# Optimization experiments

Measured on AMD Instinct MI355X. Metric: run time of the kernel, lower is better.

The kernel has to match this reference:

```python
import jax, jax.numpy as jnp
import numpy as np

K = 3  # kernel_dim
PAD = 1


def setup_inputs() -> dict:
    key = jax.random.key(0)
    ks = jax.random.split(key, 7)
    B, C_in, C_out, R = 2, 32, 64, 64
    H = W = D = 64
    return {
        "x": jax.random.normal(ks[0], (B, C_in, H, W, D), dtype=jnp.float32),
        "U_k_h": jax.random.normal(ks[1], (K, R), dtype=jnp.float32),
        "U_k_w": jax.random.normal(ks[2], (K, R), dtype=jnp.float32),
        "U_k_d": jax.random.normal(ks[3], (K, R), dtype=jnp.float32),
        "U_c_in": jax.random.normal(ks[4], (C_in, R), dtype=jnp.float32),
        "U_c_out": jax.random.normal(ks[5], (R, C_out), dtype=jnp.float32),
        "bias": jax.random.normal(ks[6], (C_out,), dtype=jnp.float32),
    }


def _cpd_conv3d(x, U_k_h, U_k_w, U_k_d, U_c_in, U_c_out, bias):
    # Equivalent to: patches[b,c,h,w,d,kh,kw,kd] contracted with
    # U_c_in[c,r] U_k_h[kh,r] U_k_w[kw,r] U_k_d[kd,r] U_c_out[r,co]
    # -> out[b,co,h,w,d].  We exploit the CP (rank-separable) structure
    # instead of materializing the unfolded patch tensor.
    xp = jnp.pad(x, ((0, 0), (0, 0), (PAD, PAD), (PAD, PAD), (PAD, PAD)))
    # channel contraction: [B, R, H+2, W+2, D+2]
    t = jnp.einsum('bchwd,cr->brhwd', xp, U_c_in)
    B, R, Hp, Wp, Dp = t.shape
    H, W, D = Hp - 2 * PAD, Wp - 2 * PAD, Dp - 2 * PAD
    # separable kernel contractions (fixed K=3 unrolled loops)
    t = sum(t[:, :, k:k + H, :, :] * U_k_h[k][None, :, None, None, None] for k in range(K))
    t = sum(t[:, :, :, k:k + W, :] * U_k_w[k][None, :, None, None, None] for k in range(K))
    t = sum(t[:, :, :, :, k:k + D] * U_k_d[k][None, :, None, None, None] for k in range(K))
    out = jnp.einsum('brhwd,rc->bchwd', t, U_c_out)
    return out + bias[None, :, None, None, None]


def reference(x, U_k_h, U_k_w, U_k_d, U_c_in, U_c_out, bias):
    return _cpd_conv3d(x, U_k_h, U_k_w, U_k_d, U_c_in, U_c_out, bias)
```

## Files before the change

### kernel.cpp

```cpp
#include <hip/hip_runtime.h>
#include <hip/hip_bf16.h>

typedef __attribute__((ext_vector_type(8))) short short8;
typedef __attribute__((ext_vector_type(4))) float f32x4;

__device__ __forceinline__ float b2f(short s) {
    return __uint_as_float(((unsigned int)(unsigned short)s) << 16);
}
__device__ __forceinline__ short f2b(float f) {
    unsigned int u = __float_as_uint(f);
    u += 0x7fffu + ((u >> 16) & 1u);
    return (short)(u >> 16);
}
__device__ __forceinline__ unsigned pack2(float a, float b) {
    return (unsigned)(unsigned short)f2b(a) | ((unsigned)(unsigned short)f2b(b) << 16);
}

__global__ __launch_bounds__(256)
void k1_channel(const float* __restrict__ x,
                const float* __restrict__ Ucin,
                short* __restrict__ t)
{
    __shared__ float xs[128 * 36];
    const int tid  = threadIdx.x;
    const int bid  = blockIdx.x;
    const int b    = bid >> 11;
    const int sp0  = (bid & 2047) << 7;
    const float* xb = x + ((long)b << 23) + sp0;

    const int lane = tid & 63;
    const int wv   = tid >> 6;

    float u[32];
#pragma unroll
    for (int c = 0; c < 32; ++c) u[c] = Ucin[c * 64 + lane];

    for (int i = tid; i < 2048; i += 256) {
        int c2 = i >> 7;
        int so = i & 127;
        float a0 = xb[((long)(2 * c2)     << 18) + so];
        float a1 = xb[((long)(2 * c2 + 1) << 18) + so];
        float2 v; v.x = a0; v.y = a1;
        *(float2*)&xs[so * 36 + 2 * c2] = v;
    }
    __syncthreads();

    short* tb = t + (((size_t)b << 18) + sp0) * 64 + lane;
    for (int s = 0; s < 32; ++s) {
        const int so = wv * 32 + s;
        const float4* row = (const float4*)&xs[so * 36];
        float a0 = 0.f, a1 = 0.f;
#pragma unroll
        for (int k = 0; k < 8; ++k) {
            float4 xx = row[k];
            a0 += xx.x * u[4 * k + 0];
            a1 += xx.y * u[4 * k + 1];
            a0 += xx.z * u[4 * k + 2];
            a1 += xx.w * u[4 * k + 3];
        }
        tb[(size_t)so * 64] = f2b(a0 + a1);
    }
}

__global__ __launch_bounds__(256)
void k2_conv_gemm(const short* __restrict__ t,
                  const float* __restrict__ Ukh,
                  const float* __restrict__ Ukw,
                  const float* __restrict__ Ukd,
                  const float* __restrict__ Uco,
                  const float* __restrict__ bias,
                  float* __restrict__ out)
{
    __shared__ short s[66 * 64];
    __shared__ short p[64 * 72];
    __shared__ short ucot[64 * 72];

    const int tid = threadIdx.x;

    const int bid  = blockIdx.x;
    const int slot = bid & 7;
    const int idx  = bid >> 3;
    const int b    = idx >> 9;
    const int rem  = idx & 511;
    const int h    = slot * 8 + (rem >> 6);
    const int w    = rem & 63;

    const short* colp[9];
    bool valid[9];
#pragma unroll
    for (int kh = 0; kh < 3; ++kh) {
#pragma unroll
        for (int kw = 0; kw < 3; ++kw) {
            int hh = h + kh - 1, ww = w + kw - 1;
            bool v = ((unsigned)hh < 64u) && ((unsigned)ww < 64u);
            valid[kh * 3 + kw] = v;
            long base = v ? ((long)(b * 262144 + hh * 4096 + ww * 64) << 6) : 0;
            colp[kh * 3 + kw] = t + base;
        }
    }

    for (int i = tid; i < 4096; i += 256) {
        int r = i >> 6, co = i & 63;
        ucot[co * 72 + r] = f2b(Uco[i]);
    }

    const int rq = tid & 15;
    float4 W[9];
    {
        float4 a[3], c[3];
#pragma unroll
        for (int k = 0; k < 3; ++k) {
            a[k] = *(const float4*)&Ukh[k * 64 + 4 * rq];
            c[k] = *(const float4*)&Ukw[k * 64 + 4 * rq];
        }
#pragma unroll
        for (int kh = 0; kh < 3; ++kh)
#pragma unroll
            for (int kw = 0; kw < 3; ++kw) {
                int kk = kh * 3 + kw;
                float m = valid[kk] ? 1.f : 0.f;
                W[kk].x = a[kh].x * c[kw].x * m;
                W[kk].y = a[kh].y * c[kw].y * m;
                W[kk].z = a[kh].z * c[kw].z * m;
                W[kk].w = a[kh].w * c[kw].w * m;
            }
    }
    for (int it = tid; it < 66 * 16; it += 256) {
        int sd = it >> 4;
        int d  = sd - 1;
        float a0 = 0.f, a1 = 0.f, a2 = 0.f, a3 = 0.f;
        if ((unsigned)d < 64u) {
            int off = d * 64 + 4 * rq;
#pragma unroll
            for (int kk = 0; kk < 9; ++kk) {
                uint2 uu = *(const uint2*)(colp[kk] + off);
                a0 += W[kk].x * b2f((short)(uu.x));
                a1 += W[kk].y * b2f((short)(uu.x >> 16));
                a2 += W[kk].z * b2f((short)(uu.y));
                a3 += W[kk].w * b2f((short)(uu.y >> 16));
            }
        }
        uint2 o; o.x = pack2(a0, a1); o.y = pack2(a2, a3);
        *(uint2*)&s[sd * 64 + 4 * rq] = o;
    }
    __syncthreads();

    {
        float4 Wd[3];
#pragma unroll
        for (int k = 0; k < 3; ++k)
            Wd[k] = *(const float4*)&Ukd[k * 64 + 4 * rq];
        for (int u = tid; u < 64 * 16; u += 256) {
            int d = u >> 4;
            float a0 = 0.f, a1 = 0.f, a2 = 0.f, a3 = 0.f;
#pragma unroll
            for (int k = 0; k < 3; ++k) {
                uint2 uu = *(const uint2*)&s[(d + k) * 64 + 4 * rq];
                a0 += Wd[k].x * b2f((short)(uu.x));
                a1 += Wd[k].y * b2f((short)(uu.x >> 16));
                a2 += Wd[k].z * b2f((short)(uu.y));
                a3 += Wd[k].w * b2f((short)(uu.y >> 16));
            }
            uint2 o; o.x = pack2(a0, a1); o.y = pack2(a2, a3);
            *(uint2*)&p[d * 72 + 4 * rq] = o;
        }
    }
    __syncthreads();

    {
        const int lane = tid & 63, wv = tid >> 6;
        const int l15 = lane & 15, quad = lane >> 4;
        short8 afr0 = *(const short8*)&p[(wv * 16 + l15) * 72 + quad * 8];
        short8 afr1 = *(const short8*)&p[(wv * 16 + l15) * 72 + 32 + quad * 8];
        f32x4 acc[4] = {};
#pragma unroll
        for (int nt = 0; nt < 4; ++nt) {
            short8 b0 = *(const short8*)&ucot[(nt * 16 + l15) * 72 + quad * 8];
            short8 b1 = *(const short8*)&ucot[(nt * 16 + l15) * 72 + 32 + quad * 8];
            acc[nt] = __builtin_amdgcn_mfma_f32_16x16x32_bf16(afr0, b0, acc[nt], 0, 0, 0);
            acc[nt] = __builtin_amdgcn_mfma_f32_16x16x32_bf16(afr1, b1, acc[nt], 0, 0, 0);
        }
#pragma unroll
        for (int nt = 0; nt < 4; ++nt) {
            int co = nt * 16 + l15;
            float bs = bias[co];
            int d = wv * 16 + quad * 4;
            float4 o;
            o.x = acc[nt][0] + bs; o.y = acc[nt][1] + bs;
            o.z = acc[nt][2] + bs; o.w = acc[nt][3] + bs;
            long addr = ((long)(b * 64 + co) << 18) + (h << 12) + (w << 6) + d;
            *(float4*)&out[addr] = o;
        }
    }
}

#define NTH 512
#define NPADP 656
#define SMEM_BYTES ((NPADP*32 + NPADP*32 + 432*32 + 64*32 + 64*64)*2 + 576*4)

__global__ __launch_bounds__(NTH)
void cpd_conv3d_fused_fb(const float* __restrict__ x,
                         const float* __restrict__ Ukh,
                         const float* __restrict__ Ukw,
                         const float* __restrict__ Ukd,
                         const float* __restrict__ Ucin,
                         const float* __restrict__ Uco,
                         const float* __restrict__ bias,
                         float* __restrict__ out)
{
    extern __shared__ char smem[];
    short* xs   = (short*)smem;
    short* t0   = xs   + NPADP*32;
    short* t1   = t0   + NPADP*32;
    short* uct  = t1   + 432*32;
    short* ucot = uct  + 64*32;
    float* ukf  = (float*)(ucot + 64*64);

    const int tid  = threadIdx.x;
    const int lane = tid & 63;
    const int wv   = tid >> 6;
    const int l15  = lane & 15;
    const int quad = lane >> 4;
    const int rg   = tid & 3;

    const int bid = blockIdx.x;
    const int dt = bid & 3, wt = (bid >> 2) & 15, ht = (bid >> 6) & 15, b = bid >> 10;
    const int h0 = ht * 4, w0 = wt * 4, d0 = dt * 16;

    for (int i = tid; i < 576; i += NTH) {
        float v = (i < 192) ? Ukh[i] : (i < 384 ? Ukw[i - 192] : Ukd[i - 384]);
        ukf[i] = v;
    }
    for (int i = tid; i < 2048; i += NTH) {
        int r = i >> 5, c = i & 31;
        uct[i] = f2b(Ucin[c * 64 + r]);
    }
    for (int i = tid; i < 4096; i += NTH) {
        int co = i >> 6, r = i & 63;
        ucot[i] = f2b(Uco[r * 64 + co]);
    }
    for (int i = tid; i < NPADP * 32; i += NTH) {
        int pp = i >> 5, c = i & 31;
        float v = 0.f;
        if (pp < 648) {
            int ph = pp / 108, rem = pp - ph * 108;
            int pw = rem / 18, pd = rem - pw * 18;
            int gh = h0 + ph - 1, gw = w0 + pw - 1, gd = d0 + pd - 1;
            if ((unsigned)gh < 64u && (unsigned)gw < 64u && (unsigned)gd < 64u)
                v = x[((long)(b * 32 + c) << 18) + (gh << 12) + (gw << 6) + gd];
        }
        xs[i] = f2b(v);
    }
    __syncthreads();

    f32x4 acc[8] = {};

    for (int pass = 0; pass < 2; ++pass) {
        const int rbase = pass * 32;
        {
            const int nt = wv & 1;
            short8 bfrag = *(const short8*)&uct[(rbase + nt * 16 + l15) * 32 + quad * 8];
            for (int mt = (wv >> 1); mt <= 40; mt += 4) {
                short8 afrag = *(const short8*)&xs[(mt * 16 + l15) * 32 + quad * 8];
                f32x4 c = {};
                c = __builtin_amdgcn_mfma_f32_16x16x32_bf16(afrag, bfrag, c, 0, 0, 0);
                const int col = nt * 16 + l15;
#pragma unroll
                for (int i2 = 0; i2 < 4; ++i2)
                    t0[(mt * 16 + quad * 4 + i2) * 32 + col] = f2b(c[i2]);
            }
        }
        __syncthreads();
        {
            float wh[3][8];
#pragma unroll
            for (int k = 0; k < 3; ++k) {
                const float4* pp_ = (const float4*)&ukf[k * 64 + rbase + rg * 8];
                float4 u0 = pp_[0], u1 = pp_[1];
                wh[k][0]=u0.x; wh[k][1]=u0.y; wh[k][2]=u0.z; wh[k][3]=u0.w;
                wh[k][4]=u1.x; wh[k][5]=u1.y; wh[k][6]=u1.z; wh[k][7]=u1.w;
            }
            for (int item = tid; item < 1728; item += NTH) {
                int q = item >> 2;
                float v[8] = {};
#pragma unroll
                for (int k = 0; k < 3; ++k) {
                    short8 sv = *(const short8*)&t0[(q + k * 108) * 32 + rg * 8];
#pragma unroll
                    for (int j = 0; j < 8; ++j) v[j] += wh[k][j] * b2f(sv[j]);
                }
                short8 o;
#pragma unroll
                for (int j = 0; j < 8; ++j) o[j] = f2b(v[j]);
                *(short8*)&t1[q * 32 + rg * 8] = o;
            }
        }
        __syncthreads();
        {
            float ww[3][8];
#pragma unroll
            for (int k = 0; k < 3; ++k) {
                const float4* pp_ = (const float4*)&ukf[(3 + k) * 64 + rbase + rg * 8];
                float4 u0 = pp_[0], u1 = pp_[1];
                ww[k][0]=u0.x; ww[k][1]=u0.y; ww[k][2]=u0.z; ww[k][3]=u0.w;
                ww[k][4]=u1.x; ww[k][5]=u1.y; ww[k][6]=u1.z; ww[k][7]=u1.w;
            }
            for (int item = tid; item < 1152; item += NTH) {
                int q2 = item >> 2;
                int oh = q2 / 72;
                int src = q2 + oh * 36;
                float v[8] = {};
#pragma unroll
                for (int k = 0; k < 3; ++k) {
                    short8 sv = *(const short8*)&t1[(src + k * 18) * 32 + rg * 8];
#pragma unroll
                    for (int j = 0; j < 8; ++j) v[j] += ww[k][j] * b2f(sv[j]);
                }
                short8 o;
#pragma unroll
                for (int j = 0; j < 8; ++j) o[j] = f2b(v[j]);
                *(short8*)&t0[q2 * 32 + rg * 8] = o;
            }
        }
        __syncthreads();
        {
            float wd[3][8];
#pragma unroll
            for (int k = 0; k < 3; ++k) {
                const float4* pp_ = (const float4*)&ukf[(6 + k) * 64 + rbase + rg * 8];
                float4 u0 = pp_[0], u1 = pp_[1];
                wd[k][0]=u0.x; wd[k][1]=u0.y; wd[k][2]=u0.z; wd[k][3]=u0.w;
                wd[k][4]=u1.x; wd[k][5]=u1.y; wd[k][6]=u1.z; wd[k][7]=u1.w;
            }
            for (int item = tid; item < 1024; item += NTH) {
                int pq = item >> 2;
                int src = pq + (pq >> 4) * 2;
                float v[8] = {};
#pragma unroll
                for (int k = 0; k < 3; ++k) {
                    short8 sv = *(const short8*)&t0[(src + k) * 32 + rg * 8];
#pragma unroll
                    for (int j = 0; j < 8; ++j) v[j] += wd[k][j] * b2f(sv[j]);
                }
                short8 o;
#pragma unroll
                for (int j = 0; j < 8; ++j) o[j] = f2b(v[j]);
                *(short8*)&t1[pq * 32 + rg * 8] = o;
            }
        }
        __syncthreads();
        {
            short8 bfr[4];
#pragma unroll
            for (int nt = 0; nt < 4; ++nt)
                bfr[nt] = *(const short8*)&ucot[(nt * 16 + l15) * 64 + rbase + quad * 8];
#pragma unroll
            for (int i = 0; i < 8; ++i) {
                int mt = wv * 2 + (i >> 2), nt = i & 3;
                short8 afr = *(const short8*)&t1[(mt * 16 + l15) * 32 + quad * 8];
                acc[i] = __builtin_amdgcn_mfma_f32_16x16x32_bf16(afr, bfr[nt], acc[i], 0, 0, 0);
            }
        }
    }

#pragma unroll
    for (int i = 0; i < 8; ++i) {
        int mt = wv * 2 + (i >> 2), nt = i & 3;
        int co = nt * 16 + l15;
        int oh = mt >> 2, ow = mt & 3;
        float bs = bias[co];
        float4 o4;
        o4.x = acc[i][0] + bs; o4.y = acc[i][1] + bs;
        o4.z = acc[i][2] + bs; o4.w = acc[i][3] + bs;
        long addr = ((long)(b * 64 + co) << 18) + ((long)(h0 + oh) << 12)
                  + ((w0 + ow) << 6) + (d0 + quad * 4);
        *(float4*)&out[addr] = o4;
    }
}

extern "C" void kernel_launch(void* const* d_in, const int* in_sizes, int n_in,
                              void* d_out, int out_size, void* d_ws, size_t ws_size,
                              hipStream_t stream) {
    const float* x    = (const float*)d_in[0];
    const float* Ukh  = (const float*)d_in[1];
    const float* Ukw  = (const float*)d_in[2];
    const float* Ukd  = (const float*)d_in[3];
    const float* Ucin = (const float*)d_in[4];
    const float* Uco  = (const float*)d_in[5];
    const float* bias = (const float*)d_in[6];
    float* out = (float*)d_out;

    const size_t needed = (size_t)2 * 262144 * 64 * 2;
    if (ws_size >= needed) {
        short* t = (short*)d_ws;
        k1_channel<<<4096, 256, 0, stream>>>(x, Ucin, t);
        k2_conv_gemm<<<8192, 256, 0, stream>>>(t, Ukh, Ukw, Ukd, Uco, bias, out);
    } else {
        (void)hipFuncSetAttribute((const void*)cpd_conv3d_fused_fb,
                                  hipFuncAttributeMaxDynamicSharedMemorySize,
                                  SMEM_BYTES);
        cpd_conv3d_fused_fb<<<2048, NTH, SMEM_BYTES, stream>>>(
            x, Ukh, Ukw, Ukd, Ucin, Uco, bias, out);
    }
}
```

Baseline: 292.5 us.

## Precompute bf16 transposed U_c_out once and software-pipeline k2 HW-stage loads

Adds a tiny prep kernel that converts and transposes U_c_out into bf16 in workspace once, so each of the 8192 k2 blocks copies it with 16-byte vector loads instead of converting 4096 floats with strided stores. The HW-combine stage is restructured into a fixed 4-iteration loop with register double-buffering of the nine column loads, and zero halo rows are written separately. This aims to hide global load latency and trim per-block setup, at the cost of more registers and an extra launch.

```diff
diff --git a/kernel.cpp b/kernel.cpp
--- a/kernel.cpp
+++ b/kernel.cpp
@@ -14,6 +14,14 @@
 }
 __device__ __forceinline__ unsigned pack2(float a, float b) {
     return (unsigned)(unsigned short)f2b(a) | ((unsigned)(unsigned short)f2b(b) << 16);
+}
+
+__global__ __launch_bounds__(64)
+void k0_prep(const float* __restrict__ Uco, short* __restrict__ ucotT)
+{
+    const int i  = blockIdx.x * 64 + threadIdx.x;
+    const int co = i >> 6, r = i & 63;
+    ucotT[co * 64 + r] = f2b(Uco[r * 64 + co]);
 }
 
 __global__ __launch_bounds__(256)
@@ -69,6 +77,7 @@
                   const float* __restrict__ Ukd,
                   const float* __restrict__ Uco,
                   const float* __restrict__ bias,
+                  const short* __restrict__ ucotT,
                   float* __restrict__ out)
 {
     __shared__ short s[66 * 64];
@@ -99,9 +108,17 @@
         }
     }
 
-    for (int i = tid; i < 4096; i += 256) {
-        int r = i >> 6, co = i & 63;
-        ucot[co * 72 + r] = f2b(Uco[i]);
+    if (ucotT) {
+        for (int i = tid; i < 512; i += 256) {
+            int co = i >> 3, rb = i & 7;
+            short8 v = *(const short8*)&ucotT[co * 64 + rb * 8];
+            *(short8*)&ucot[co * 72 + rb * 8] = v;
+        }
+    } else {
+        for (int i = tid; i < 4096; i += 256) {
+            int r = i >> 6, co = i & 63;
+            ucot[co * 72 + r] = f2b(Uco[i]);
+        }
     }
 
     const int rq = tid & 15;
@@ -125,23 +142,46 @@
                 W[kk].w = a[kh].w * c[kw].w * m;
             }
     }
-    for (int it = tid; it < 66 * 16; it += 256) {
-        int sd = it >> 4;
-        int d  = sd - 1;
-        float a0 = 0.f, a1 = 0.f, a2 = 0.f, a3 = 0.f;
-        if ((unsigned)d < 64u) {
-            int off = d * 64 + 4 * rq;
+
+    if (tid < 32) {
+        int sd = (tid < 16) ? 0 : 65;
+        int rr = tid & 15;
+        uint2 z; z.x = 0u; z.y = 0u;
+        *(uint2*)&s[sd * 64 + 4 * rr] = z;
+    }
+
+    {
+        const int off0 = (tid >> 4) * 64 + 4 * rq;
+        uint2 cur[9];
+#pragma unroll
+        for (int kk = 0; kk < 9; ++kk)
+            cur[kk] = *(const uint2*)(colp[kk] + off0);
+
+#pragma unroll
+        for (int j = 0; j < 4; ++j) {
+            uint2 nxt[9];
+            if (j < 3) {
+#pragma unroll
+                for (int kk = 0; kk < 9; ++kk)
+                    nxt[kk] = *(const uint2*)(colp[kk] + off0 + 1024 * (j + 1));
+            }
+            float a0 = 0.f, a1 = 0.f, a2 = 0.f, a3 = 0.f;
 #pragma unroll
             for (int kk = 0; kk < 9; ++kk) {
-                uint2 uu = *(const uint2*)(colp[kk] + off);
+                uint2 uu = cur[kk];
                 a0 += W[kk].x * b2f((short)(uu.x));
                 a1 += W[kk].y * b2f((short)(uu.x >> 16));
                 a2 += W[kk].z * b2f((short)(uu.y));
                 a3 += W[kk].w * b2f((short)(uu.y >> 16));
             }
-        }
-        uint2 o; o.x = pack2(a0, a1); o.y = pack2(a2, a3);
-        *(uint2*)&s[sd * 64 + 4 * rq] = o;
+            int sd = 1 + (tid >> 4) + 16 * j;
+            uint2 o; o.x = pack2(a0, a1); o.y = pack2(a2, a3);
+            *(uint2*)&s[sd * 64 + 4 * rq] = o;
+            if (j < 3) {
+#pragma unroll
+                for (int kk = 0; kk < 9; ++kk) cur[kk] = nxt[kk];
+            }
+        }
     }
     __syncthreads();
 
@@ -390,11 +430,17 @@
     const float* bias = (const float*)d_in[6];
     float* out = (float*)d_out;
 
-    const size_t needed = (size_t)2 * 262144 * 64 * 2;
-    if (ws_size >= needed) {
+    const size_t needT = (size_t)2 * 262144 * 64 * 2;
+    const size_t needM = 4096 * 2;
+    if (ws_size >= needT) {
         short* t = (short*)d_ws;
+        short* ucotT = nullptr;
+        if (ws_size >= needT + needM) {
+            ucotT = (short*)((char*)d_ws + needT);
+            k0_prep<<<64, 64, 0, stream>>>(Uco, ucotT);
+        }
         k1_channel<<<4096, 256, 0, stream>>>(x, Ucin, t);
-        k2_conv_gemm<<<8192, 256, 0, stream>>>(t, Ukh, Ukw, Ukd, Uco, bias, out);
+        k2_conv_gemm<<<8192, 256, 0, stream>>>(t, Ukh, Ukw, Ukd, Uco, bias, ucotT, out);
     } else {
         (void)hipFuncSetAttribute((const void*)cpd_conv3d_fused_fb,
                                   hipFuncAttributeMaxDynamicSharedMemorySize,
```

After: 277.2 us. 1.06x faster.
